# Kernel tuning notes

Hardware: AMD Instinct MI355X
Metric: run time of the kernel (lower is better)

The kernel has to match this reference:

```python
import jax, jax.numpy as jnp
import numpy as np

B, N = 128, 1024

def setup_inputs() -> dict:
    key = jax.random.key(0)
    inputs = jax.random.normal(key, (B, N), dtype=jnp.float32)
    return {"inputs": inputs}

def reference(inputs) -> jnp.ndarray:
    # Per sample a: meshgrid(a, a) -> x[i,j]=a[j], y[i,j]=a[i]; x - y = a[j]-a[i].
    # boolean_mask with strict upper triangle (j > i), row-major order.
    n = inputs.shape[1]
    diff = inputs[:, None, :] - inputs[:, :, None]  # [B, n, n], diff[b,i,j]=a[b,j]-a[b,i]
    rows, cols = jnp.triu_indices(n, k=1)           # row-major upper-triangle order
    return diff[:, rows, cols]                      # [B, n*(n-1)//2]
```

## Files before the change

### kernel.cpp

```cpp
#include <hip/hip_runtime.h>


#define NPOS 1024
#define PAIRS ((NPOS * (NPOS - 1)) / 2)

__global__ __launch_bounds__(256) void relpos_kernel(const float* __restrict__ in,
                                                     float* __restrict__ out) {
    const int nRows = NPOS - 1;
    const int bid = blockIdx.x;
    const int b = bid / nRows;
    const int i = bid - b * nRows;

    const float* __restrict__ a = in + b * NPOS;
    const float ai = a[i];

    const int rowStart = b * PAIRS + i * nRows - (i * (i - 1)) / 2;
    const int cnt = nRows - i;
    float* __restrict__ o = out + rowStart;
    const float* __restrict__ src = a + i + 1;

    const int tid = threadIdx.x;

    int head = (4 - (rowStart & 3)) & 3;
    if (head > cnt) head = cnt;
    if (tid < head) o[tid] = src[tid] - ai;

    const int nvec = (cnt - head) >> 2;
    for (int v = tid; v < nvec; v += 256) {
        const int t = head + (v << 2);
        float4 r;
        r.x = src[t]     - ai;
        r.y = src[t + 1] - ai;
        r.z = src[t + 2] - ai;
        r.w = src[t + 3] - ai;
        *reinterpret_cast<float4*>(o + t) = r;
    }

    const int t2 = head + (nvec << 2) + tid;
    if (t2 < cnt) o[t2] = src[t2] - ai;
}

extern "C" void kernel_launch(void* const* d_in, const int* in_sizes, int n_in,
                              void* d_out, int out_size, void* d_ws, size_t ws_size,
                              hipStream_t stream) {
    const float* in = (const float*)d_in[0];
    float* out = (float*)d_out;
    const int B = in_sizes[0] / NPOS;
    const dim3 grid(B * (NPOS - 1));
    relpos_kernel<<<grid, 256, 0, stream>>>(in, out);
}
```

Before: 302.8 us.

## Split output into fixed equal chunks with closed-form row lookup per element

Replaces the one-block-per-row launch, whose blocks have very uneven work, with 32 equal-size chunks per batch. Each thread maps its flat output index back to (i,j) with a sqrt-based inverse of the triangular index plus correction loops. This balances load and reduces block count, and PAIRS is a multiple of 4, so every float4 store is aligned. The cost is extra per-element index arithmetic and gathered input reads; output stores are fully aligned and coalesced.

```diff
diff --git a/kernel.cpp b/kernel.cpp
--- a/kernel.cpp
+++ b/kernel.cpp
@@ -1,43 +1,58 @@
 #include <hip/hip_runtime.h>
+#include <math.h>
 
 
-#define NPOS 1024
-#define PAIRS ((NPOS * (NPOS - 1)) / 2)
+#define NPOS  1024
+#define PAIRS 523776
+#define CHUNK 16368
+#define CHUNKS_PER_BATCH 32
+#define F4_PER_CHUNK (CHUNK / 4)
+
+__device__ __forceinline__ int rowStartOf(int i) {
+    return (i * (2 * NPOS - 1 - i)) >> 1;
+}
+
+__device__ __forceinline__ int row_of(int p) {
+    const float D = (float)(4190209 - 8 * p);
+    int i = (int)((2047.0f - sqrtf(D)) * 0.5f);
+    if (i < 0) i = 0;
+    if (i > NPOS - 2) i = NPOS - 2;
+    while (rowStartOf(i + 1) <= p) ++i;
+    while (rowStartOf(i) > p) --i;
+    return i;
+}
 
 __global__ __launch_bounds__(256) void relpos_kernel(const float* __restrict__ in,
                                                      float* __restrict__ out) {
-    const int nRows = NPOS - 1;
-    const int bid = blockIdx.x;
-    const int b = bid / nRows;
-    const int i = bid - b * nRows;
+    const int b = blockIdx.x / CHUNKS_PER_BATCH;
+    const int c = blockIdx.x - b * CHUNKS_PER_BATCH;
 
     const float* __restrict__ a = in + b * NPOS;
-    const float ai = a[i];
+    float* __restrict__ ob = out + b * PAIRS;
+    const int chunkBase = c * CHUNK;
 
-    const int rowStart = b * PAIRS + i * nRows - (i * (i - 1)) / 2;
-    const int cnt = nRows - i;
-    float* __restrict__ o = out + rowStart;
-    const float* __restrict__ src = a + i + 1;
-
-    const int tid = threadIdx.x;
-
-    int head = (4 - (rowStart & 3)) & 3;
-    if (head > cnt) head = cnt;
-    if (tid < head) o[tid] = src[tid] - ai;
-
-    const int nvec = (cnt - head) >> 2;
-    for (int v = tid; v < nvec; v += 256) {
-        const int t = head + (v << 2);
-        float4 r;
-        r.x = src[t]     - ai;
-        r.y = src[t + 1] - ai;
-        r.z = src[t + 2] - ai;
-        r.w = src[t + 3] - ai;
-        *reinterpret_cast<float4*>(o + t) = r;
+    for (int v = threadIdx.x; v < F4_PER_CHUNK; v += 256) {
+        const int p = chunkBase + (v << 2);
+        const int i = row_of(p);
+        const int j = i + 1 + (p - rowStartOf(i));
+        if (j + 3 <= NPOS - 1) {
+            const float ai = a[i];
+            float4 r;
+            r.x = a[j]     - ai;
+            r.y = a[j + 1] - ai;
+            r.z = a[j + 2] - ai;
+            r.w = a[j + 3] - ai;
+            *reinterpret_cast<float4*>(ob + p) = r;
+        } else {
+            #pragma unroll
+            for (int e = 0; e < 4; ++e) {
+                const int pe = p + e;
+                const int ie = row_of(pe);
+                const int je = ie + 1 + (pe - rowStartOf(ie));
+                ob[pe] = a[je] - a[ie];
+            }
+        }
     }
-
-    const int t2 = head + (nvec << 2) + tid;
-    if (t2 < cnt) o[t2] = src[t2] - ai;
 }
 
 extern "C" void kernel_launch(void* const* d_in, const int* in_sizes, int n_in,
@@ -46,6 +61,5 @@
     const float* in = (const float*)d_in[0];
     float* out = (float*)d_out;
     const int B = in_sizes[0] / NPOS;
-    const dim3 grid(B * (NPOS - 1));
-    relpos_kernel<<<grid, 256, 0, stream>>>(in, out);
+    relpos_kernel<<<dim3(B * CHUNKS_PER_BATCH), 256, 0, stream>>>(in, out);
 }
```

Result: faster. 282.7 us (-6.6%).
